# Kernel tuning notes

Measured on AMD Instinct MI355X. Metric: run time of the kernel, lower is better.

Reference implementation:

```python
import jax, jax.numpy as jnp
import numpy as np

I, H, O = 32, 64, 8  # input_size, hidden_layer, output_size
B, T = 4096, 256


def setup_inputs() -> dict:
    key = jax.random.key(0)
    ks = jax.random.split(key, 7)
    s_ih = 1.0 / np.sqrt(H)
    return {
        "x": jax.random.normal(ks[0], (B, T, I), dtype=jnp.float32),
        # PyTorch nn.LSTM params, gate order [i, f, g, o]
        "W_ih": jax.random.uniform(ks[1], (4 * H, I), jnp.float32, -s_ih, s_ih),
        "W_hh": jax.random.uniform(ks[2], (4 * H, H), jnp.float32, -s_ih, s_ih),
        "b_ih": jax.random.uniform(ks[3], (4 * H,), jnp.float32, -s_ih, s_ih),
        "b_hh": jax.random.uniform(ks[4], (4 * H,), jnp.float32, -s_ih, s_ih),
        "W_fc": jax.random.uniform(ks[5], (O, H), jnp.float32, -s_ih, s_ih),
        "b_fc": jax.random.uniform(ks[6], (O,), jnp.float32, -s_ih, s_ih),
    }


def reference(x, W_ih, W_hh, b_ih, b_hh, W_fc, b_fc):
    # Precompute input-to-hidden projections for all timesteps in one GEMM.
    # [B, T, 4H]
    x_proj = jnp.einsum('bti,gi->btg', x, W_ih) + b_ih + b_hh

    def step(carry, xp_t):
        h, c = carry  # [B, H] each
        gates = xp_t + h @ W_hh.T  # [B, 4H]
        i_g, f_g, g_g, o_g = jnp.split(gates, 4, axis=-1)
        i_g = jax.nn.sigmoid(i_g)
        f_g = jax.nn.sigmoid(f_g)
        g_g = jnp.tanh(g_g)
        o_g = jax.nn.sigmoid(o_g)
        c = f_g * c + i_g * g_g
        h = o_g * jnp.tanh(c)
        return (h, c), None

    h0 = jnp.zeros((x.shape[0], H), dtype=x.dtype)
    c0 = jnp.zeros((x.shape[0], H), dtype=x.dtype)
    # scan over time axis: move T to leading axis
    (h_T, c_T), _ = jax.lax.scan(step, (h0, c0), jnp.swapaxes(x_proj, 0, 1))
    # out[:, -1, :] == final hidden state for single-layer batch_first LSTM
    return h_T @ W_fc.T + b_fc
```

## Files before the change

### kernel.cpp

```cpp
#include <hip/hip_runtime.h>
#include <hip/hip_bf16.h>


#define T_LEN 256
#define I_SZ  32
#define H_SZ  64
#define O_SZ  8
#define BR    16
#define HS    72

typedef __attribute__((ext_vector_type(8))) short short8;
typedef __attribute__((ext_vector_type(4))) float f32x4;

static __device__ __forceinline__ unsigned fbits(float f) {
    union { float f; unsigned u; } v; v.f = f; return v.u;
}
static __device__ __forceinline__ unsigned pk2t(float lo, float hi) {
    return __builtin_amdgcn_perm(fbits(hi), fbits(lo), 0x07060302u);
}
static __device__ __forceinline__ short f2bf_rne(float f) {
    union { __hip_bfloat16 b; short s; } u;
    u.b = __float2bfloat16(f);
    return u.s;
}
static __device__ __forceinline__ f32x4 rcp4(f32x4 d) {
    f32x4 r;
    r.x = __builtin_amdgcn_rcpf(d.x);
    r.y = __builtin_amdgcn_rcpf(d.y);
    r.z = __builtin_amdgcn_rcpf(d.z);
    r.w = __builtin_amdgcn_rcpf(d.w);
    return r;
}
static __device__ __forceinline__ f32x4 exp2_4(f32x4 m) {
    f32x4 e;
    e.x = __builtin_amdgcn_exp2f(m.x);
    e.y = __builtin_amdgcn_exp2f(m.y);
    e.z = __builtin_amdgcn_exp2f(m.z);
    e.w = __builtin_amdgcn_exp2f(m.w);
    return e;
}
static __device__ __forceinline__ f32x4 clamp4(f32x4 x, float lo, float hi) {
    f32x4 r;
    r.x = __builtin_amdgcn_fmed3f(x.x, lo, hi);
    r.y = __builtin_amdgcn_fmed3f(x.y, lo, hi);
    r.z = __builtin_amdgcn_fmed3f(x.z, lo, hi);
    r.w = __builtin_amdgcn_fmed3f(x.w, lo, hi);
    return r;
}
static __device__ __forceinline__ f32x4 fma4(f32x4 a, f32x4 b, f32x4 c) {
    return __builtin_elementwise_fma(a, b, c);
}

#define LOG2E     1.4426950408889634f
#define TWO_LOG2E 2.8853900817779268f
#define ECLAMP    28.8f

__global__ __launch_bounds__(256, 1)
void lstm_fused_kernel(const float* __restrict__ x,
                       const float* __restrict__ W_ih,
                       const float* __restrict__ W_hh,
                       const float* __restrict__ b_ih,
                       const float* __restrict__ b_hh,
                       const float* __restrict__ W_fc,
                       const float* __restrict__ b_fc,
                       float* __restrict__ out)
{
    __shared__ short hbuf[2][BR][HS];
    __shared__ float Hf[BR][64];

    const int tid   = threadIdx.x;
    const int wave  = tid >> 6;
    const int lane  = tid & 63;
    const int quad  = lane >> 4;
    const int nlow  = lane & 15;
    const int jw    = wave * 16 + nlow;
    const int rbase = quad * 4;
    const int b0    = blockIdx.x * BR;

    short8 bfrag[4][3];
    f32x4  biasf[4];
    for (int g = 0; g < 4; ++g) {
        const float scale = (g == 2) ? -TWO_LOG2E : -LOG2E;
        const int col = g * 64 + jw;
        {
            const float* wr = W_ih + col * I_SZ + quad * 8;
            short8 f;
            #pragma unroll
            for (int e = 0; e < 8; ++e) f[e] = f2bf_rne(scale * wr[e]);
            bfrag[g][0] = f;
        }
        #pragma unroll
        for (int kt = 1; kt < 3; ++kt) {
            const float* wr = W_hh + col * H_SZ + (kt - 1) * 32 + quad * 8;
            short8 f;
            #pragma unroll
            for (int e = 0; e < 8; ++e) f[e] = f2bf_rne(scale * wr[e]);
            bfrag[g][kt] = f;
        }
        const float bg = scale * (b_ih[col] + b_hh[col]);
        biasf[g] = (f32x4){bg, bg, bg, bg};
    }

    for (int q = tid; q < 2 * BR * HS; q += 256) ((short*)hbuf)[q] = (short)0;

    const float* xb = x + ((size_t)(b0 + nlow) * T_LEN) * I_SZ + quad * 8;

    float4 nx[16];
    short8 sc[8];
    #pragma unroll
    for (int s = 0; s < 8; ++s) {
        nx[2*s]   = *(const float4*)(xb + s * I_SZ);
        nx[2*s+1] = *(const float4*)(xb + s * I_SZ + 4);
    }
    #pragma unroll
    for (int s = 0; s < 8; ++s) {
        union { uint4 u; short8 v; } w;
        w.u.x = pk2t(nx[2*s].x,   nx[2*s].y);
        w.u.y = pk2t(nx[2*s].z,   nx[2*s].w);
        w.u.z = pk2t(nx[2*s+1].x, nx[2*s+1].y);
        w.u.w = pk2t(nx[2*s+1].z, nx[2*s+1].w);
        sc[s] = w.v;
    }

    const short* rb[2] = { &hbuf[0][nlow][quad * 8], &hbuf[1][nlow][quad * 8] };
    short*       wb[2] = { &hbuf[0][rbase][jw],      &hbuf[1][rbase][jw] };

    f32x4 cc = {0.f, 0.f, 0.f, 0.f};
    f32x4 hh = {0.f, 0.f, 0.f, 0.f};

    f32x4 preacc[4];
    #pragma unroll
    for (int g = 0; g < 4; ++g)
        preacc[g] = __builtin_amdgcn_mfma_f32_16x16x32_bf16(sc[0], bfrag[g][0], biasf[g], 0, 0, 0);

    for (int ch = 0; ch < 32; ++ch) {
        #pragma unroll
        for (int tc = 0; tc < 8; ++tc) {
            const int t = ch * 8 + tc;

            __syncthreads();

            const short* hr = rb[t & 1];
            short8 a1 = *(const short8*)(hr);
            short8 a2 = *(const short8*)(hr + 32);

            if (tc == 0 && ch + 1 < 32) {
                const float* nxt = xb + (t + 8) * I_SZ;
                #pragma unroll
                for (int s = 0; s < 8; ++s) {
                    nx[2*s]   = *(const float4*)(nxt + s * I_SZ);
                    nx[2*s+1] = *(const float4*)(nxt + s * I_SZ + 4);
                }
            }

            f32x4 acc[4];
            #pragma unroll
            for (int g = 0; g < 4; ++g) {
                f32x4 a = __builtin_amdgcn_mfma_f32_16x16x32_bf16(a1, bfrag[g][1], preacc[g], 0, 0, 0);
                a = __builtin_amdgcn_mfma_f32_16x16x32_bf16(a2, bfrag[g][2], a, 0, 0, 0);
                acc[g] = a;
            }

            if (tc == 7 && ch + 1 < 32) {
                #pragma unroll
                for (int s = 0; s < 8; ++s) {
                    union { uint4 u; short8 v; } w;
                    w.u.x = pk2t(nx[2*s].x,   nx[2*s].y);
                    w.u.y = pk2t(nx[2*s].z,   nx[2*s].w);
                    w.u.z = pk2t(nx[2*s+1].x, nx[2*s+1].y);
                    w.u.w = pk2t(nx[2*s+1].z, nx[2*s+1].w);
                    sc[s] = w.v;
                }
            }

            const short8 nax = sc[(tc + 1) & 7];
            #pragma unroll
            for (int g = 0; g < 4; ++g)
                preacc[g] = __builtin_amdgcn_mfma_f32_16x16x32_bf16(nax, bfrag[g][0], biasf[g], 0, 0, 0);

            f32x4 ei = exp2_4(acc[0]);
            f32x4 ef = exp2_4(acc[1]);
            f32x4 eg = exp2_4(clamp4(acc[2], -ECLAMP, ECLAMP));
            f32x4 eo = exp2_4(acc[3]);
            f32x4 fv = rcp4(ef + 1.0f);
            f32x4 ig = (1.0f - eg) * rcp4((ei + 1.0f) * (eg + 1.0f));
            cc = fma4(fv, cc, ig);
            f32x4 ec = exp2_4(clamp4(cc * (-TWO_LOG2E), -ECLAMP, ECLAMP));
            hh = (1.0f - ec) * rcp4((eo + 1.0f) * (ec + 1.0f));

            short* hw = wb[(t + 1) & 1];
            hw[0 * HS] = (short)((fbits(hh.x) + 0x8000u) >> 16);
            hw[1 * HS] = (short)((fbits(hh.y) + 0x8000u) >> 16);
            hw[2 * HS] = (short)((fbits(hh.z) + 0x8000u) >> 16);
            hw[3 * HS] = (short)((fbits(hh.w) + 0x8000u) >> 16);
        }
    }

    Hf[rbase + 0][jw] = hh.x;
    Hf[rbase + 1][jw] = hh.y;
    Hf[rbase + 2][jw] = hh.z;
    Hf[rbase + 3][jw] = hh.w;
    __syncthreads();

    if (tid < BR * O_SZ) {
        const int r = tid >> 3;
        const int o = tid & 7;
        const float* wf = W_fc + o * H_SZ;
        float acc = b_fc[o];
        #pragma unroll
        for (int jx = 0; jx < H_SZ; ++jx) acc += Hf[r][jx] * wf[jx];
        out[(size_t)(b0 + r) * O_SZ + o] = acc;
    }
}

extern "C" void kernel_launch(void* const* d_in, const int* in_sizes, int n_in,
                              void* d_out, int out_size, void* d_ws, size_t ws_size,
                              hipStream_t stream) {
    const float* x    = (const float*)d_in[0];
    const float* W_ih = (const float*)d_in[1];
    const float* W_hh = (const float*)d_in[2];
    const float* b_ih = (const float*)d_in[3];
    const float* b_hh = (const float*)d_in[4];
    const float* W_fc = (const float*)d_in[5];
    const float* b_fc = (const float*)d_in[6];
    float* out = (float*)d_out;

    const int B = 4096;
    lstm_fused_kernel<<<dim3(B / BR), dim3(256), 0, stream>>>(
        x, W_ih, W_hh, b_ih, b_hh, W_fc, b_fc, out);
}
```

Before: 282.1 us.

## Split LSTM gates across twice as many waves with shared-memory gate exchange

Doubles the block to 512 threads. Each wave pair splits the four gates: one half computes the i/f gate MFMAs and the other the g/o gates, and they exchange half their accumulators through shared memory so each thread runs the activations for two rows instead of four. The aim is to shorten the serial per-timestep critical path (MFMA chain plus transcendental work) by spreading it over more waves. In exchange it adds a second __syncthreads per timestep and LDS traffic for the exchange.

After: 355.1 us. 25.9% more time.

```diff
diff --git a/kernel.cpp b/kernel.cpp
--- a/kernel.cpp
+++ b/kernel.cpp
@@ -11,6 +11,7 @@
 
 typedef __attribute__((ext_vector_type(8))) short short8;
 typedef __attribute__((ext_vector_type(4))) float f32x4;
+typedef __attribute__((ext_vector_type(2))) float f32x2;
 
 static __device__ __forceinline__ unsigned fbits(float f) {
     union { float f; unsigned u; } v; v.f = f; return v.u;
@@ -23,31 +24,25 @@
     u.b = __float2bfloat16(f);
     return u.s;
 }
-static __device__ __forceinline__ f32x4 rcp4(f32x4 d) {
-    f32x4 r;
+static __device__ __forceinline__ f32x2 rcp2(f32x2 d) {
+    f32x2 r;
     r.x = __builtin_amdgcn_rcpf(d.x);
     r.y = __builtin_amdgcn_rcpf(d.y);
-    r.z = __builtin_amdgcn_rcpf(d.z);
-    r.w = __builtin_amdgcn_rcpf(d.w);
     return r;
 }
-static __device__ __forceinline__ f32x4 exp2_4(f32x4 m) {
-    f32x4 e;
+static __device__ __forceinline__ f32x2 exp2_2(f32x2 m) {
+    f32x2 e;
     e.x = __builtin_amdgcn_exp2f(m.x);
     e.y = __builtin_amdgcn_exp2f(m.y);
-    e.z = __builtin_amdgcn_exp2f(m.z);
-    e.w = __builtin_amdgcn_exp2f(m.w);
     return e;
 }
-static __device__ __forceinline__ f32x4 clamp4(f32x4 x, float lo, float hi) {
-    f32x4 r;
+static __device__ __forceinline__ f32x2 clamp2(f32x2 x, float lo, float hi) {
+    f32x2 r;
     r.x = __builtin_amdgcn_fmed3f(x.x, lo, hi);
     r.y = __builtin_amdgcn_fmed3f(x.y, lo, hi);
-    r.z = __builtin_amdgcn_fmed3f(x.z, lo, hi);
-    r.w = __builtin_amdgcn_fmed3f(x.w, lo, hi);
     return r;
 }
-static __device__ __forceinline__ f32x4 fma4(f32x4 a, f32x4 b, f32x4 c) {
+static __device__ __forceinline__ f32x2 fma2(f32x2 a, f32x2 b, f32x2 c) {
     return __builtin_elementwise_fma(a, b, c);
 }
 
@@ -55,7 +50,7 @@
 #define TWO_LOG2E 2.8853900817779268f
 #define ECLAMP    28.8f
 
-__global__ __launch_bounds__(256, 1)
+__global__ __launch_bounds__(512, 1)
 void lstm_fused_kernel(const float* __restrict__ x,
                        const float* __restrict__ W_ih,
                        const float* __restrict__ W_hh,
@@ -67,19 +62,25 @@
 {
     __shared__ short hbuf[2][BR][HS];
     __shared__ float Hf[BR][64];
+    __shared__ f32x4 xch[2][4][64];
 
     const int tid   = threadIdx.x;
     const int wave  = tid >> 6;
     const int lane  = tid & 63;
     const int quad  = lane >> 4;
     const int nlow  = lane & 15;
-    const int jw    = wave * 16 + nlow;
+    const int pair  = wave & 3;
+    const int half  = wave >> 2;
+    const int jw    = pair * 16 + nlow;
     const int rbase = quad * 4;
+    const int myr   = rbase + half * 2;
     const int b0    = blockIdx.x * BR;
 
-    short8 bfrag[4][3];
-    f32x4  biasf[4];
-    for (int g = 0; g < 4; ++g) {
+    short8 bfrag[2][3];
+    f32x2  biasf2[2];
+    f32x4  biasf[2];
+    for (int gg = 0; gg < 2; ++gg) {
+        const int g = half * 2 + gg;
         const float scale = (g == 2) ? -TWO_LOG2E : -LOG2E;
         const int col = g * 64 + jw;
         {
@@ -87,7 +88,7 @@
             short8 f;
             #pragma unroll
             for (int e = 0; e < 8; ++e) f[e] = f2bf_rne(scale * wr[e]);
-            bfrag[g][0] = f;
+            bfrag[gg][0] = f;
         }
         #pragma unroll
         for (int kt = 1; kt < 3; ++kt) {
@@ -95,13 +96,15 @@
             short8 f;
             #pragma unroll
             for (int e = 0; e < 8; ++e) f[e] = f2bf_rne(scale * wr[e]);
-            bfrag[g][kt] = f;
+            bfrag[gg][kt] = f;
         }
         const float bg = scale * (b_ih[col] + b_hh[col]);
-        biasf[g] = (f32x4){bg, bg, bg, bg};
-    }
-
-    for (int q = tid; q < 2 * BR * HS; q += 256) ((short*)hbuf)[q] = (short)0;
+        biasf[gg] = (f32x4){bg, bg, bg, bg};
+        biasf2[gg] = (f32x2){bg, bg};
+        (void)biasf2;
+    }
+
+    for (int q = tid; q < 2 * BR * HS; q += 512) ((short*)hbuf)[q] = (short)0;
 
     const float* xb = x + ((size_t)(b0 + nlow) * T_LEN) * I_SZ + quad * 8;
 
@@ -123,15 +126,15 @@
     }
 
     const short* rb[2] = { &hbuf[0][nlow][quad * 8], &hbuf[1][nlow][quad * 8] };
-    short*       wb[2] = { &hbuf[0][rbase][jw],      &hbuf[1][rbase][jw] };
-
-    f32x4 cc = {0.f, 0.f, 0.f, 0.f};
-    f32x4 hh = {0.f, 0.f, 0.f, 0.f};
-
-    f32x4 preacc[4];
+    short*       wb[2] = { &hbuf[0][myr][jw],        &hbuf[1][myr][jw] };
+
+    f32x2 cc = {0.f, 0.f};
+    f32x2 hh = {0.f, 0.f};
+
+    f32x4 preacc[2];
     #pragma unroll
-    for (int g = 0; g < 4; ++g)
-        preacc[g] = __builtin_amdgcn_mfma_f32_16x16x32_bf16(sc[0], bfrag[g][0], biasf[g], 0, 0, 0);
+    for (int gg = 0; gg < 2; ++gg)
+        preacc[gg] = __builtin_amdgcn_mfma_f32_16x16x32_bf16(sc[0], bfrag[gg][0], biasf[gg], 0, 0, 0);
 
     for (int ch = 0; ch < 32; ++ch) {
         #pragma unroll
@@ -153,13 +156,18 @@
                 }
             }
 
-            f32x4 acc[4];
-            #pragma unroll
-            for (int g = 0; g < 4; ++g) {
-                f32x4 a = __builtin_amdgcn_mfma_f32_16x16x32_bf16(a1, bfrag[g][1], preacc[g], 0, 0, 0);
-                a = __builtin_amdgcn_mfma_f32_16x16x32_bf16(a2, bfrag[g][2], a, 0, 0, 0);
-                acc[g] = a;
-            }
+            f32x4 acc[2];
+            #pragma unroll
+            for (int gg = 0; gg < 2; ++gg) {
+                f32x4 a = __builtin_amdgcn_mfma_f32_16x16x32_bf16(a1, bfrag[gg][1], preacc[gg], 0, 0, 0);
+                a = __builtin_amdgcn_mfma_f32_16x16x32_bf16(a2, bfrag[gg][2], a, 0, 0, 0);
+                acc[gg] = a;
+            }
+
+            f32x4 send;
+            if (half == 0) send = (f32x4){acc[0].z, acc[0].w, acc[1].z, acc[1].w};
+            else           send = (f32x4){acc[0].x, acc[0].y, acc[1].x, acc[1].y};
+            xch[half][pair][lane] = send;
 
             if (tc == 7 && ch + 1 < 32) {
                 #pragma unroll
@@ -175,31 +183,44 @@
 
             const short8 nax = sc[(tc + 1) & 7];
             #pragma unroll
-            for (int g = 0; g < 4; ++g)
-                preacc[g] = __builtin_amdgcn_mfma_f32_16x16x32_bf16(nax, bfrag[g][0], biasf[g], 0, 0, 0);
-
-            f32x4 ei = exp2_4(acc[0]);
-            f32x4 ef = exp2_4(acc[1]);
-            f32x4 eg = exp2_4(clamp4(acc[2], -ECLAMP, ECLAMP));
-            f32x4 eo = exp2_4(acc[3]);
-            f32x4 fv = rcp4(ef + 1.0f);
-            f32x4 ig = (1.0f - eg) * rcp4((ei + 1.0f) * (eg + 1.0f));
-            cc = fma4(fv, cc, ig);
-            f32x4 ec = exp2_4(clamp4(cc * (-TWO_LOG2E), -ECLAMP, ECLAMP));
-            hh = (1.0f - ec) * rcp4((eo + 1.0f) * (ec + 1.0f));
+            for (int gg = 0; gg < 2; ++gg)
+                preacc[gg] = __builtin_amdgcn_mfma_f32_16x16x32_bf16(nax, bfrag[gg][0], biasf[gg], 0, 0, 0);
+
+            __syncthreads();
+
+            const f32x4 r = xch[half ^ 1][pair][lane];
+
+            f32x2 pi, pf, pg, po;
+            if (half == 0) {
+                pi = (f32x2){acc[0].x, acc[0].y};
+                pf = (f32x2){acc[1].x, acc[1].y};
+                pg = (f32x2){r.x, r.y};
+                po = (f32x2){r.z, r.w};
+            } else {
+                pi = (f32x2){r.x, r.y};
+                pf = (f32x2){r.z, r.w};
+                pg = (f32x2){acc[0].z, acc[0].w};
+                po = (f32x2){acc[1].z, acc[1].w};
+            }
+
+            f32x2 ei = exp2_2(pi);
+            f32x2 ef = exp2_2(pf);
+            f32x2 eg = exp2_2(clamp2(pg, -ECLAMP, ECLAMP));
+            f32x2 eo = exp2_2(po);
+            f32x2 fv = rcp2(ef + 1.0f);
+            f32x2 ig = (1.0f - eg) * rcp2((ei + 1.0f) * (eg + 1.0f));
+            cc = fma2(fv, cc, ig);
+            f32x2 ec = exp2_2(clamp2(cc * (-TWO_LOG2E), -ECLAMP, ECLAMP));
+            hh = (1.0f - ec) * rcp2((eo + 1.0f) * (ec + 1.0f));
 
             short* hw = wb[(t + 1) & 1];
-            hw[0 * HS] = (short)((fbits(hh.x) + 0x8000u) >> 16);
-            hw[1 * HS] = (short)((fbits(hh.y) + 0x8000u) >> 16);
-            hw[2 * HS] = (short)((fbits(hh.z) + 0x8000u) >> 16);
-            hw[3 * HS] = (short)((fbits(hh.w) + 0x8000u) >> 16);
+            hw[0]  = (short)((fbits(hh.x) + 0x8000u) >> 16);
+            hw[HS] = (short)((fbits(hh.y) + 0x8000u) >> 16);
         }
     }
 
-    Hf[rbase + 0][jw] = hh.x;
-    Hf[rbase + 1][jw] = hh.y;
-    Hf[rbase + 2][jw] = hh.z;
-    Hf[rbase + 3][jw] = hh.w;
+    Hf[myr + 0][jw] = hh.x;
+    Hf[myr + 1][jw] = hh.y;
     __syncthreads();
 
     if (tid < BR * O_SZ) {
@@ -226,6 +247,6 @@
     float* out = (float*)d_out;
 
     const int B = 4096;
-    lstm_fused_kernel<<<dim3(B / BR), dim3(256), 0, stream>>>(
+    lstm_fused_kernel<<<dim3(B / BR), dim3(512), 0, stream>>>(
         x, W_ih, W_hh, b_ih, b_hh, W_fc, b_fc, out);
 }
```

## Permute hidden-state LDS rows and spread x conversion across timesteps

Applied to the files above, without the earlier changes.

The hidden-state buffer rows are written and read through a permuted row mapping (prd/pw0..3), so each lane's four h writes land at different LDS positions. The intent is to cut bank conflicts on the per-step stores and short8 loads. The next step's input-projection MFMAs are now issued before the recurrent MFMAs rather than after them. The bf16 packing of prefetched x, previously done all at once at tc==7, is spread with one slice converted per timestep. This flattens the per-step instruction mix on the serial recurrence path, at the cost of some extra registers holding preacc_n.

Result: no change. 283.8 us (+0.6%).

```diff
diff --git a/kernel.cpp b/kernel.cpp
--- a/kernel.cpp
+++ b/kernel.cpp
@@ -77,6 +77,12 @@
     const int rbase = quad * 4;
     const int b0    = blockIdx.x * BR;
 
+    const int prd = 2 * (nlow >> 2) + 8 * (nlow & 1) + ((nlow >> 1) & 1);
+    const int pw0 = 2 * quad + 0;
+    const int pw1 = 2 * quad + 8;
+    const int pw2 = 2 * quad + 1;
+    const int pw3 = 2 * quad + 9;
+
     short8 bfrag[4][3];
     f32x4  biasf[4];
     for (int g = 0; g < 4; ++g) {
@@ -122,8 +128,8 @@
         sc[s] = w.v;
     }
 
-    const short* rb[2] = { &hbuf[0][nlow][quad * 8], &hbuf[1][nlow][quad * 8] };
-    short*       wb[2] = { &hbuf[0][rbase][jw],      &hbuf[1][rbase][jw] };
+    const short* rb[2] = { &hbuf[0][prd][quad * 8], &hbuf[1][prd][quad * 8] };
+    short*       wb[2] = { &hbuf[0][0][jw],         &hbuf[1][0][jw] };
 
     f32x4 cc = {0.f, 0.f, 0.f, 0.f};
     f32x4 hh = {0.f, 0.f, 0.f, 0.f};
@@ -144,14 +150,28 @@
             short8 a1 = *(const short8*)(hr);
             short8 a2 = *(const short8*)(hr + 32);
 
-            if (tc == 0 && ch + 1 < 32) {
-                const float* nxt = xb + (t + 8) * I_SZ;
-                #pragma unroll
-                for (int s = 0; s < 8; ++s) {
-                    nx[2*s]   = *(const float4*)(nxt + s * I_SZ);
-                    nx[2*s+1] = *(const float4*)(nxt + s * I_SZ + 4);
+            if (tc == 0) {
+                union { uint4 u; short8 v; } w;
+                w.u.x = pk2t(nx[14].x, nx[14].y);
+                w.u.y = pk2t(nx[14].z, nx[14].w);
+                w.u.z = pk2t(nx[15].x, nx[15].y);
+                w.u.w = pk2t(nx[15].z, nx[15].w);
+                sc[7] = w.v;
+                if (ch + 1 < 32) {
+                    const float* nxt = xb + (t + 8) * I_SZ;
+                    #pragma unroll
+                    for (int s = 0; s < 8; ++s) {
+                        nx[2*s]   = *(const float4*)(nxt + s * I_SZ);
+                        nx[2*s+1] = *(const float4*)(nxt + s * I_SZ + 4);
+                    }
                 }
             }
+
+            const short8 nax = sc[(tc + 1) & 7];
+            f32x4 preacc_n[4];
+            #pragma unroll
+            for (int g = 0; g < 4; ++g)
+                preacc_n[g] = __builtin_amdgcn_mfma_f32_16x16x32_bf16(nax, bfrag[g][0], biasf[g], 0, 0, 0);
 
             f32x4 acc[4];
             #pragma unroll
@@ -161,22 +181,18 @@
                 acc[g] = a;
             }
 
-            if (tc == 7 && ch + 1 < 32) {
-                #pragma unroll
-                for (int s = 0; s < 8; ++s) {
-                    union { uint4 u; short8 v; } w;
-                    w.u.x = pk2t(nx[2*s].x,   nx[2*s].y);
-                    w.u.y = pk2t(nx[2*s].z,   nx[2*s].w);
-                    w.u.z = pk2t(nx[2*s+1].x, nx[2*s+1].y);
-                    w.u.w = pk2t(nx[2*s+1].z, nx[2*s+1].w);
-                    sc[s] = w.v;
-                }
+            if (tc >= 1) {
+                const int s = tc - 1;
+                union { uint4 u; short8 v; } w;
+                w.u.x = pk2t(nx[2*s].x,   nx[2*s].y);
+                w.u.y = pk2t(nx[2*s].z,   nx[2*s].w);
+                w.u.z = pk2t(nx[2*s+1].x, nx[2*s+1].y);
+                w.u.w = pk2t(nx[2*s+1].z, nx[2*s+1].w);
+                sc[s] = w.v;
             }
 
-            const short8 nax = sc[(tc + 1) & 7];
-            #pragma unroll
-            for (int g = 0; g < 4; ++g)
-                preacc[g] = __builtin_amdgcn_mfma_f32_16x16x32_bf16(nax, bfrag[g][0], biasf[g], 0, 0, 0);
+            #pragma unroll
+            for (int g = 0; g < 4; ++g) preacc[g] = preacc_n[g];
 
             f32x4 ei = exp2_4(acc[0]);
             f32x4 ef = exp2_4(acc[1]);
@@ -189,10 +205,10 @@
             hh = (1.0f - ec) * rcp4((eo + 1.0f) * (ec + 1.0f));
 
             short* hw = wb[(t + 1) & 1];
-            hw[0 * HS] = (short)((fbits(hh.x) + 0x8000u) >> 16);
-            hw[1 * HS] = (short)((fbits(hh.y) + 0x8000u) >> 16);
-            hw[2 * HS] = (short)((fbits(hh.z) + 0x8000u) >> 16);
-            hw[3 * HS] = (short)((fbits(hh.w) + 0x8000u) >> 16);
+            hw[pw0 * HS] = (short)((fbits(hh.x) + 0x8000u) >> 16);
+            hw[pw1 * HS] = (short)((fbits(hh.y) + 0x8000u) >> 16);
+            hw[pw2 * HS] = (short)((fbits(hh.z) + 0x8000u) >> 16);
+            hw[pw3 * HS] = (short)((fbits(hh.w) + 0x8000u) >> 16);
         }
     }
 
```
